# Kernel tuning notes

Hardware: AMD Instinct MI355X
Metric: run time of the kernel (lower is better)

## Reference

```python
import jax, jax.numpy as jnp
import numpy as np

N = 100000
D = 256
E = 1600000
H, C = 2, 32  # heads, out_channels


def setup_inputs() -> dict:
    key = jax.random.key(0)
    ks = jax.random.split(key, 10)
    h_x = jax.random.normal(ks[0], (N, D), dtype=jnp.float32)
    t_x = jax.random.normal(ks[1], (N, D), dtype=jnp.float32)
    src = jax.random.randint(ks[2], (E,), 0, N, dtype=jnp.int32)
    off = jax.random.randint(ks[3], (E,), 1, N, dtype=jnp.int32)
    dst = (src + off) % N  # guarantees src != dst (remove_self_loops is a no-op)
    edge_index = jnp.stack([src, dst])  # [2, E]
    enrichment_weights = jax.random.uniform(ks[4], (E,), dtype=jnp.float32) * 3.0
    s = 1.0 / np.sqrt(D)
    W_src = jax.random.normal(ks[5], (D, H * C), dtype=jnp.float32) * s
    W_dst = jax.random.normal(ks[6], (D, H * C), dtype=jnp.float32) * s
    att_src = jax.random.normal(ks[7], (H, C), dtype=jnp.float32) * 0.1
    att_dst = jax.random.normal(ks[8], (H, C), dtype=jnp.float32) * 0.1
    bias = jnp.zeros((H * C,), dtype=jnp.float32)
    enrichment_scale = jnp.float32(0.5)
    return {"h_x": h_x, "t_x": t_x, "edge_index": edge_index,
            "enrichment_weights": enrichment_weights,
            "W_src": W_src, "W_dst": W_dst, "att_src": att_src,
            "att_dst": att_dst, "bias": bias,
            "enrichment_scale": enrichment_scale}


def _gat(x_src, x_dst, src, dst, num_dst, W_src, W_dst, att_src, att_dst, bias):
    # PyG GATConv, bipartite, heads=H, out=C, concat=True, eval mode
    hs = (x_src @ W_src).reshape(-1, H, C)  # [Ns, H, C]
    hd = (x_dst @ W_dst).reshape(-1, H, C)  # [Nd, H, C]
    a_s = jnp.einsum('nhc,hc->nh', hs, att_src)  # [Ns, H]
    a_d = jnp.einsum('nhc,hc->nh', hd, att_dst)  # [Nd, H]
    alpha = jax.nn.leaky_relu(a_s[src] + a_d[dst], 0.2)  # [E', H]
    m = jax.ops.segment_max(alpha, dst, num_segments=num_dst)
    alpha = jnp.exp(alpha - m[dst])
    z = jax.ops.segment_sum(alpha, dst, num_segments=num_dst)
    alpha = alpha / (z[dst] + 1e-16)
    msg = hs[src] * alpha[:, :, None]  # [E', H, C]
    out = jax.ops.segment_sum(msg, dst, num_segments=num_dst)  # [Nd, H, C]
    return out.reshape(num_dst, H * C) + bias


def reference(h_x, t_x, edge_index, enrichment_weights,
              W_src, W_dst, att_src, att_dst, bias, enrichment_scale):
    h_in = jax.nn.elu(h_x)
    t_in = jax.nn.elu(t_x)
    src, dst = edge_index[0], edge_index[1]
    loops = jnp.arange(min(h_x.shape[0], t_x.shape[0]), dtype=src.dtype)
    # direction 1: (h -> t), PyG appends self-loops after the input edges
    s1 = jnp.concatenate([src, loops]); d1 = jnp.concatenate([dst, loops])
    t_rep = _gat(h_in, t_in, s1, d1, t_x.shape[0], W_src, W_dst, att_src, att_dst, bias)
    # direction 2: reversed edges (t -> h)
    s2 = jnp.concatenate([dst, loops]); d2 = jnp.concatenate([src, loops])
    h_rep = _gat(t_in, h_in, s2, d2, h_x.shape[0], W_src, W_dst, att_src, att_dst, bias)
    # edge-enrichment reweighting (scalar factor)
    scale = 0.5 * jnp.tanh(enrichment_scale)
    ew = jnp.clip(enrichment_weights, 0.3, 3.0)
    aw = jax.nn.softmax(ew)
    weighted = jnp.sum(aw * ew)
    factor = 1.0 + scale * (weighted - 1.0)
    return (h_rep * factor, t_rep * factor)
```

## Files before the change

kernel.cpp:

```cpp
#include <hip/hip_runtime.h>
#include <hip/hip_fp16.h>
#include <math.h>

typedef __attribute__((ext_vector_type(8))) short bf16x8;
typedef __attribute__((ext_vector_type(4))) float f32x4;

__device__ __forceinline__ float bf2f(unsigned short u) {
    union { unsigned int i; float f; } c;
    c.i = ((unsigned int)u) << 16;
    return c.f;
}
__device__ __forceinline__ unsigned short f2bf(float f) {
    union { float f; unsigned int i; } c;
    c.f = f;
    unsigned int b = c.i + 0x7FFFu + ((c.i >> 16) & 1u);
    return (unsigned short)(b >> 16);
}
__device__ __forceinline__ float eluf(float v) {
    return v > 0.f ? v : (__expf(v) - 1.f);
}
__device__ __forceinline__ float lrelu(float v) {
    return v >= 0.f ? v : 0.2f * v;
}
__device__ __forceinline__ unsigned int fenc(float f) {
    union { float f; unsigned int u; } c; c.f = f;
    return (c.u & 0x80000000u) ? ~c.u : (c.u | 0x80000000u);
}
__device__ __forceinline__ float fdec(unsigned int k) {
    union { float f; unsigned int u; } c;
    c.u = (k & 0x80000000u) ? (k ^ 0x80000000u) : ~k;
    return c.f;
}

__global__ void detect_kernel(const unsigned int* __restrict__ w, int nwords,
                              int* __restrict__ flag)
{
    __shared__ int cnt_s;
    if (threadIdx.x == 0) cnt_s = 0;
    __syncthreads();
    int sane = 0;
    for (int i = threadIdx.x; i < nwords; i += 256) {
        unsigned int lo = w[i] & 0xffffu;
        int e = (int)((lo >> 7) & 0xffu);
        if (e >= 114 && e <= 136) sane++;
    }
    atomicAdd(&cnt_s, sane);
    __syncthreads();
    if (threadIdx.x == 0) *flag = (2 * cnt_s > nwords) ? 1 : 0;
}

__global__ __launch_bounds__(256) void wfrag_kernel(
    const unsigned short* __restrict__ Wsrc, const unsigned short* __restrict__ Wdst,
    const int* __restrict__ flag, unsigned short* __restrict__ Wfrag)
{
    if (!*flag) return;
    const int nch = 8 * 8 * 64;
    for (int ch = blockIdx.x * 256 + threadIdx.x; ch < nch; ch += gridDim.x * 256) {
        int l  = ch & 63;
        int t  = (ch >> 6) & 7;
        int ks = ch >> 9;
        int col = t * 16 + (l & 15);
        int k0  = ks * 32 + (l >> 4) * 8;
        const unsigned short* W = (col < 64) ? (Wsrc + col) : (Wdst + (col - 64));
#pragma unroll
        for (int j = 0; j < 8; ++j)
            Wfrag[(size_t)ch * 8 + j] = W[(size_t)(k0 + j) * 64];
    }
}

__global__ __launch_bounds__(256) void gemm_mfma_kernel(
    const void* __restrict__ xh, const void* __restrict__ xt,
    const unsigned short* __restrict__ Wfrag,
    const void* __restrict__ att_src, const void* __restrict__ att_dst,
    const int* __restrict__ flag,
    __half* __restrict__ P, float* __restrict__ as_all, float* __restrict__ ad_all,
    int N)
{
    if (!*flag) return;
    const unsigned short* xv = (const unsigned short*)((blockIdx.y == 0) ? xh : xt);
    __half* Pout = P + (size_t)blockIdx.y * (size_t)N * 64u;
    float* asO  = as_all + (size_t)blockIdx.y * (size_t)N * 2u;
    float* adO  = ad_all + (size_t)blockIdx.y * (size_t)N * 2u;
    const int tid = threadIdx.x;
    const int w   = tid >> 6;
    const int l   = tid & 63;
    const int l15 = l & 15;
    const int lhi = l >> 4;
    const int rowA = blockIdx.x * 64 + w * 16 + l15;
    const bool rv = rowA < N;

    bf16x8 a[8];
#pragma unroll
    for (int ks = 0; ks < 8; ++ks) {
        union { bf16x8 v; unsigned int u[4]; } o;
        if (rv) {
            uint4 raw = *(const uint4*)(xv + (size_t)rowA * 256 + ks * 32 + lhi * 8);
            unsigned int wsr[4] = {raw.x, raw.y, raw.z, raw.w};
#pragma unroll
            for (int i = 0; i < 4; ++i) {
                float lo = eluf(bf2f((unsigned short)(wsr[i] & 0xffffu)));
                float hi = eluf(bf2f((unsigned short)(wsr[i] >> 16)));
                o.u[i] = (unsigned int)f2bf(lo) | ((unsigned int)f2bf(hi) << 16);
            }
        } else {
            o.u[0] = o.u[1] = o.u[2] = o.u[3] = 0u;
        }
        a[ks] = o.v;
    }

    f32x4 acc[8];
#pragma unroll
    for (int t = 0; t < 8; ++t) acc[t] = (f32x4){0.f, 0.f, 0.f, 0.f};

    const bf16x8* wf = (const bf16x8*)Wfrag;
#pragma unroll
    for (int ks = 0; ks < 8; ++ks) {
#pragma unroll
        for (int t = 0; t < 8; ++t) {
            bf16x8 b = wf[(ks * 8 + t) * 64 + l];
            acc[t] = __builtin_amdgcn_mfma_f32_16x16x32_bf16(a[ks], b, acc[t], 0, 0, 0);
        }
    }

    float asv[4], adv[4];
#pragma unroll
    for (int t = 0; t < 4; ++t) {
        asv[t] = bf2f(((const unsigned short*)att_src)[t * 16 + l15]);
        adv[t] = bf2f(((const unsigned short*)att_dst)[t * 16 + l15]);
    }
    const int rbase = blockIdx.x * 64 + w * 16 + lhi * 4;
#pragma unroll
    for (int reg = 0; reg < 4; ++reg) {
        int row = rbase + reg;
        bool ok = row < N;
        if (ok) {
            __half* p = Pout + (size_t)row * 64 + l15;
#pragma unroll
            for (int t = 0; t < 4; ++t) p[t * 16] = __float2half(acc[t][reg]);
        }
        float s0 = acc[0][reg] * asv[0] + acc[1][reg] * asv[1];
        float s1 = acc[2][reg] * asv[2] + acc[3][reg] * asv[3];
        float d0 = acc[4][reg] * adv[0] + acc[5][reg] * adv[1];
        float d1 = acc[6][reg] * adv[2] + acc[7][reg] * adv[3];
#pragma unroll
        for (int o2 = 8; o2 >= 1; o2 >>= 1) {
            s0 += __shfl_xor(s0, o2, 64);
            s1 += __shfl_xor(s1, o2, 64);
            d0 += __shfl_xor(d0, o2, 64);
            d1 += __shfl_xor(d1, o2, 64);
        }
        if (ok && l15 == 0) {
            asO[(size_t)row * 2 + 0] = s0;
            asO[(size_t)row * 2 + 1] = s1;
            adO[(size_t)row * 2 + 0] = d0;
            adO[(size_t)row * 2 + 1] = d1;
        }
    }
}

__global__ __launch_bounds__(256) void gemm_elu_kernel(
    const void* __restrict__ xh, const void* __restrict__ xt,
    const void* __restrict__ Wsrc, const void* __restrict__ Wdst,
    const void* __restrict__ att_src, const void* __restrict__ att_dst,
    const int* __restrict__ flag,
    __half* __restrict__ P, float* __restrict__ as_all, float* __restrict__ ad_all,
    int N, int D, int skip_bf)
{
    const int isbf = *flag;
    if (skip_bf && isbf) return;
    __shared__ float xs[64][33];
    __shared__ float wt[32][128];
    const void* xv = (blockIdx.y == 0) ? xh : xt;
    __half* Pout = P + (size_t)blockIdx.y * (size_t)N * 64u;
    float* asO  = as_all + (size_t)blockIdx.y * (size_t)N * 2u;
    float* adO  = ad_all + (size_t)blockIdx.y * (size_t)N * 2u;
    const int rowBase = blockIdx.x * 64;
    const int tid = threadIdx.x;
    const int tcx = tid & 15;
    const int tcy = tid >> 4;

    float acc[4][8];
#pragma unroll
    for (int r = 0; r < 4; ++r)
#pragma unroll
        for (int c = 0; c < 8; ++c) acc[r][c] = 0.f;

    for (int kc = 0; kc < D; kc += 32) {
        {
            int row = tid >> 2;
            int kq  = (tid & 3) * 8;
            int r = rowBase + row;
            float v[8];
            if (r < N) {
                if (isbf) {
                    const unsigned short* xb = (const unsigned short*)xv;
                    uint4 raw = *(const uint4*)(xb + (size_t)r * D + kc + kq);
                    unsigned int ws[4] = {raw.x, raw.y, raw.z, raw.w};
#pragma unroll
                    for (int i = 0; i < 4; ++i) {
                        v[2 * i]     = bf2f((unsigned short)(ws[i] & 0xffffu));
                        v[2 * i + 1] = bf2f((unsigned short)(ws[i] >> 16));
                    }
                } else {
                    const float* xf = (const float*)xv;
                    const float4* p4 = (const float4*)(xf + (size_t)r * D + kc + kq);
                    float4 f0 = p4[0], f1 = p4[1];
                    v[0] = f0.x; v[1] = f0.y; v[2] = f0.z; v[3] = f0.w;
                    v[4] = f1.x; v[5] = f1.y; v[6] = f1.z; v[7] = f1.w;
                }
#pragma unroll
                for (int i = 0; i < 8; ++i) v[i] = eluf(v[i]);
            } else {
#pragma unroll
                for (int i = 0; i < 8; ++i) v[i] = 0.f;
            }
#pragma unroll
            for (int i = 0; i < 8; ++i) xs[row][kq + i] = v[i];
        }
#pragma unroll
        for (int i = 0; i < 2; ++i) {
            int f = (tid + i * 256) * 8;
            int k = f >> 7;
            int c = f & 127;
            float v[8];
            if (isbf) {
                const unsigned short* Wp = (c < 64)
                    ? ((const unsigned short*)Wsrc + (size_t)(kc + k) * 64 + c)
                    : ((const unsigned short*)Wdst + (size_t)(kc + k) * 64 + (c - 64));
                uint4 raw = *(const uint4*)Wp;
                unsigned int ws[4] = {raw.x, raw.y, raw.z, raw.w};
#pragma unroll
                for (int q = 0; q < 4; ++q) {
                    v[2 * q]     = bf2f((unsigned short)(ws[q] & 0xffffu));
                    v[2 * q + 1] = bf2f((unsigned short)(ws[q] >> 16));
                }
            } else {
                const float* Wp = (c < 64)
                    ? ((const float*)Wsrc + (size_t)(kc + k) * 64 + c)
                    : ((const float*)Wdst + (size_t)(kc + k) * 64 + (c - 64));
                const float4* p4 = (const float4*)Wp;
                float4 f0 = p4[0], f1 = p4[1];
                v[0] = f0.x; v[1] = f0.y; v[2] = f0.z; v[3] = f0.w;
                v[4] = f1.x; v[5] = f1.y; v[6] = f1.z; v[7] = f1.w;
            }
#pragma unroll
            for (int q = 0; q < 8; ++q) wt[k][c + q] = v[q];
        }
        __syncthreads();
#pragma unroll 8
        for (int k = 0; k < 32; ++k) {
            float xr[4];
#pragma unroll
            for (int r = 0; r < 4; ++r) xr[r] = xs[tcy * 4 + r][k];
            float4 w0 = *(const float4*)&wt[k][tcx * 8];
            float4 w1 = *(const float4*)&wt[k][tcx * 8 + 4];
#pragma unroll
            for (int r = 0; r < 4; ++r) {
                acc[r][0] += xr[r] * w0.x; acc[r][1] += xr[r] * w0.y;
                acc[r][2] += xr[r] * w0.z; acc[r][3] += xr[r] * w0.w;
                acc[r][4] += xr[r] * w1.x; acc[r][5] += xr[r] * w1.y;
                acc[r][6] += xr[r] * w1.z; acc[r][7] += xr[r] * w1.w;
            }
        }
        __syncthreads();
    }

    float attv[8];
#pragma unroll
    for (int q = 0; q < 8; ++q) {
        int c = tcx * 8 + q;
        if (isbf) attv[q] = (c < 64) ? bf2f(((const unsigned short*)att_src)[c])
                                     : bf2f(((const unsigned short*)att_dst)[c - 64]);
        else      attv[q] = (c < 64) ? ((const float*)att_src)[c]
                                     : ((const float*)att_dst)[c - 64];
    }

#pragma unroll
    for (int r = 0; r < 4; ++r) {
        int row = rowBase + tcy * 4 + r;
        bool ok = row < N;
        if (ok && tcx < 8) {
            __half* p = Pout + (size_t)row * 64 + tcx * 8;
#pragma unroll
            for (int q = 0; q < 8; ++q) p[q] = __float2half(acc[r][q]);
        }
        float part = 0.f;
#pragma unroll
        for (int q = 0; q < 8; ++q) part += acc[r][q] * attv[q];
        part += __shfl_xor(part, 1, 64);
        part += __shfl_xor(part, 2, 64);
        if (ok && (tcx & 3) == 0) {
            if (tcx == 0)       asO[(size_t)row * 2 + 0] = part;
            else if (tcx == 4)  asO[(size_t)row * 2 + 1] = part;
            else if (tcx == 8)  adO[(size_t)row * 2 + 0] = part;
            else                adO[(size_t)row * 2 + 1] = part;
        }
    }
}

__global__ __launch_bounds__(256) void gmax_kernel(
    const float* __restrict__ as_all, unsigned int* __restrict__ gmax, int N)
{
    unsigned int k0 = 0, k1 = 0, k2 = 0, k3 = 0;
    const int total = 2 * N;
    for (int i = blockIdx.x * 256 + threadIdx.x; i < total; i += gridDim.x * 256) {
        float2 v = *(const float2*)(as_all + (size_t)i * 2);
        unsigned int ex = fenc(v.x), ey = fenc(v.y);
        if (i < N) { k0 = max(k0, ex); k1 = max(k1, ey); }
        else       { k2 = max(k2, ex); k3 = max(k3, ey); }
    }
#pragma unroll
    for (int o = 32; o >= 1; o >>= 1) {
        k0 = max(k0, (unsigned int)__shfl_xor((int)k0, o, 64));
        k1 = max(k1, (unsigned int)__shfl_xor((int)k1, o, 64));
        k2 = max(k2, (unsigned int)__shfl_xor((int)k2, o, 64));
        k3 = max(k3, (unsigned int)__shfl_xor((int)k3, o, 64));
    }
    if ((threadIdx.x & 63) == 0) {
        atomicMax(&gmax[0], k0);
        atomicMax(&gmax[1], k1);
        atomicMax(&gmax[2], k2);
        atomicMax(&gmax[3], k3);
    }
}

__global__ void count_kernel(const int* __restrict__ srce, const int* __restrict__ dste,
                             int* __restrict__ cnt, int N, int E)
{
    int e = blockIdx.x * blockDim.x + threadIdx.x;
    if (e >= E) return;
    atomicAdd(&cnt[dste[e]], 1);
    atomicAdd(&cnt[N + srce[e]], 1);
}

__global__ __launch_bounds__(256) void scan_bsum_kernel(
    const int* __restrict__ cnt, int M, int chunk, int* __restrict__ bsum)
{
    __shared__ int r[4];
    int beg = blockIdx.x * chunk;
    int end = beg + chunk; if (end > M) end = M;
    int s = 0;
    for (int i = beg + threadIdx.x; i < end; i += 256) s += cnt[i];
#pragma unroll
    for (int o = 32; o >= 1; o >>= 1) s += __shfl_down(s, o, 64);
    int lane = threadIdx.x & 63, wv = threadIdx.x >> 6;
    if (lane == 0) r[wv] = s;
    __syncthreads();
    if (threadIdx.x == 0) bsum[blockIdx.x] = r[0] + r[1] + r[2] + r[3];
}

__global__ __launch_bounds__(256) void scan_boff_kernel(
    const int* __restrict__ bsum, int NB, int* __restrict__ boff)
{
    __shared__ int s[256];
    int t = threadIdx.x;
    int v = (t < NB) ? bsum[t] : 0;
    s[t] = v;
    __syncthreads();
    for (int o = 1; o < 256; o <<= 1) {
        int x = (t >= o) ? s[t - o] : 0;
        __syncthreads();
        s[t] += x;
        __syncthreads();
    }
    if (t < NB) boff[t] = s[t] - v;
}

__global__ __launch_bounds__(256) void scan_write_kernel(
    const int* __restrict__ cnt, int M, int chunk,
    const int* __restrict__ boff, int* __restrict__ off)
{
    __shared__ int s[256];
    int t = threadIdx.x;
    int beg = blockIdx.x * chunk;
    int end = beg + chunk; if (end > M) end = M;
    if (beg >= M) return;
    int running = boff[blockIdx.x];
    for (int base = beg; base < end; base += 256) {
        int i = base + t;
        int v = (i < end) ? cnt[i] : 0;
        s[t] = v;
        __syncthreads();
        for (int o = 1; o < 256; o <<= 1) {
            int x = (t >= o) ? s[t - o] : 0;
            __syncthreads();
            s[t] += x;
            __syncthreads();
        }
        if (i < end) off[i] = running + s[t] - v;
        int total = s[255];
        __syncthreads();
        running += total;
    }
    if (end == M && t == 0) off[M] = running;
}

__global__ void fill_kernel(const int* __restrict__ srce, const int* __restrict__ dste,
                            const int* __restrict__ off, int* __restrict__ cur,
                            int* __restrict__ idx, int N, int E)
{
    int e = blockIdx.x * blockDim.x + threadIdx.x;
    if (e >= E) return;
    int s = srce[e], d = dste[e];
    int p  = atomicAdd(&cur[d], 1);
    idx[off[d] + p] = s;
    int p2 = atomicAdd(&cur[N + s], 1);
    idx[off[N + s] + p2] = d;
}

__global__ __launch_bounds__(256) void enrich_kernel(
    const void* __restrict__ ew, const int* __restrict__ flag,
    float* __restrict__ S, int E)
{
    __shared__ float r1[4], r2[4];
    const int isbf = *flag;
    float e1 = 0.f, e2 = 0.f;
    for (int i = blockIdx.x * 256 + threadIdx.x; i < E; i += gridDim.x * 256) {
        float c = isbf ? bf2f(((const unsigned short*)ew)[i]) : ((const float*)ew)[i];
        c = fminf(fmaxf(c, 0.3f), 3.0f);
        float ex = __expf(c);
        e1 += ex;
        e2 += c * ex;
    }
#pragma unroll
    for (int o = 32; o >= 1; o >>= 1) {
        e1 += __shfl_down(e1, o, 64);
        e2 += __shfl_down(e2, o, 64);
    }
    int lane = threadIdx.x & 63;
    int wv = threadIdx.x >> 6;
    if (lane == 0) { r1[wv] = e1; r2[wv] = e2; }
    __syncthreads();
    if (threadIdx.x == 0) {
        atomicAdd(&S[0], r1[0] + r1[1] + r1[2] + r1[3]);
        atomicAdd(&S[1], r2[0] + r2[1] + r2[2] + r2[3]);
    }
}

__global__ __launch_bounds__(256) void agg_kernel(
    const int* __restrict__ off, const int* __restrict__ idx,
    const float* __restrict__ as_all, const float* __restrict__ ad_all,
    const __half* __restrict__ Pall,
    const void* __restrict__ bias,
    const float* __restrict__ S,
    const unsigned int* __restrict__ gmax,
    const void* __restrict__ esc,
    const int* __restrict__ flag,
    void* __restrict__ out, int N)
{
    const int isbf = *flag;
    int q = (blockIdx.x * 256 + threadIdx.x) >> 6;
    int lane = threadIdx.x & 63;
    if (q >= 2 * N) return;
    int dir = (q >= N) ? 1 : 0;
    int n = q - dir * N;
    const float* a_s  = as_all + (size_t)dir * 2u * (size_t)N;
    const float* a_d  = ad_all + (size_t)(1 - dir) * 2u * (size_t)N;
    const __half* Psrc = Pall + (size_t)dir * (size_t)N * 64u;
    size_t outOff = dir ? 0u : (size_t)N * 64u;
    const int hi = lane >> 5;
    const int jb = off[q], je = off[q + 1];

    float2 adv2 = *(const float2*)(a_d + (size_t)n * 2);
    const float adv = hi ? adv2.y : adv2.x;
    const float gm  = fdec(gmax[dir * 2 + hi]);
    const float m   = lrelu(gm + adv);

    float2 ass2 = *(const float2*)(a_s + (size_t)n * 2);
    const float pSelf = __expf(lrelu((hi ? ass2.y : ass2.x) + adv) - m);
    float z0 = pSelf, z1 = 0.f;
    float acc0 = pSelf * __half2float(Psrc[(size_t)n * 64 + lane]);
    float acc1 = 0.f;

    int j = jb;
    for (; j + 1 < je; j += 2) {
        int s0 = idx[j], s1 = idx[j + 1];
        float2 a0 = *(const float2*)(a_s + (size_t)s0 * 2);
        float2 a1 = *(const float2*)(a_s + (size_t)s1 * 2);
        float h0 = __half2float(Psrc[(size_t)s0 * 64 + lane]);
        float h1 = __half2float(Psrc[(size_t)s1 * 64 + lane]);
        float p0 = __expf(lrelu((hi ? a0.y : a0.x) + adv) - m);
        float p1 = __expf(lrelu((hi ? a1.y : a1.x) + adv) - m);
        z0 += p0; acc0 = fmaf(p0, h0, acc0);
        z1 += p1; acc1 = fmaf(p1, h1, acc1);
    }
    if (j < je) {
        int s0 = idx[j];
        float2 a0 = *(const float2*)(a_s + (size_t)s0 * 2);
        float h0 = __half2float(Psrc[(size_t)s0 * 64 + lane]);
        float p0 = __expf(lrelu((hi ? a0.y : a0.x) + adv) - m);
        z0 += p0; acc0 = fmaf(p0, h0, acc0);
    }
    float z   = z0 + z1;
    float acc = acc0 + acc1;

    float escv = isbf ? bf2f(((const unsigned short*)esc)[0]) : ((const float*)esc)[0];
    float bv   = isbf ? bf2f(((const unsigned short*)bias)[lane]) : ((const float*)bias)[lane];
    float weighted = S[1] / S[0];
    float factor = 1.f + 0.5f * tanhf(escv) * (weighted - 1.f);
    float o = (acc / (z + 1e-16f) + bv) * factor;
    size_t oi = outOff + (size_t)n * 64 + lane;
    if (isbf) ((unsigned short*)out)[oi] = f2bf(o);
    else      ((float*)out)[oi] = o;
}

extern "C" void kernel_launch(void* const* d_in, const int* in_sizes, int n_in,
                              void* d_out, int out_size, void* d_ws, size_t ws_size,
                              hipStream_t stream)
{
    const void* hx      = d_in[0];
    const void* tx      = d_in[1];
    const int*  eidx    = (const int*)d_in[2];
    const void* ew      = d_in[3];
    const void* Wsrc    = d_in[4];
    const void* Wdst    = d_in[5];
    const void* att_src = d_in[6];
    const void* att_dst = d_in[7];
    const void* bias    = d_in[8];
    const void* esc     = d_in[9];

    const int HC = in_sizes[6];
    const int D  = in_sizes[4] / HC;
    const int N  = in_sizes[0] / D;
    const int E  = in_sizes[3];
    const int* srce = eidx;
    const int* dste = eidx + E;

    const bool canM = (D == 256) && (HC == 64);
    const int skipBf = canM ? 1 : 0;

    char* wsb = (char*)d_ws;
    size_t o = 0;
    auto alloc = [&](size_t bytes) -> void* {
        void* p = wsb + o;
        o += (bytes + 255) & ~(size_t)255;
        return p;
    };
    __half* Pall  = (__half*)alloc((size_t)2 * N * 64 * 2);
    float* as_all = (float*)alloc((size_t)2 * N * 2 * 4);
    float* ad_all = (float*)alloc((size_t)2 * N * 2 * 4);
    float* S      = (float*)alloc(2 * 4);
    unsigned int* gmax = (unsigned int*)alloc(4 * 4);
    int*   cnt    = (int*)alloc((size_t)2 * N * 4);
    int*   offp   = (int*)alloc(((size_t)2 * N + 1) * 4);
    int*   cur    = (int*)alloc((size_t)2 * N * 4);
    int*   idx    = (int*)alloc((size_t)2 * E * 4);
    int*   flag   = (int*)alloc(256);
    int*   bsum   = (int*)alloc(256 * 4);
    int*   boff   = (int*)alloc(256 * 4);
    unsigned short* Wfrag = (unsigned short*)alloc((size_t)8 * 8 * 64 * 8 * 2);

    hipMemsetAsync(cnt, 0, (size_t)2 * N * 4, stream);
    hipMemsetAsync(cur, 0, (size_t)2 * N * 4, stream);
    hipMemsetAsync(S, 0, 2 * 4, stream);
    hipMemsetAsync(gmax, 0, 4 * 4, stream);

    detect_kernel<<<1, 256, 0, stream>>>((const unsigned int*)hx, 65536, flag);

    dim3 gGemm((N + 63) / 64, 2);
    if (canM) {
        wfrag_kernel<<<16, 256, 0, stream>>>((const unsigned short*)Wsrc,
                                             (const unsigned short*)Wdst, flag, Wfrag);
        gemm_mfma_kernel<<<gGemm, 256, 0, stream>>>(hx, tx, Wfrag, att_src, att_dst,
                                                    flag, Pall, as_all, ad_all, N);
    }
    gemm_elu_kernel<<<gGemm, 256, 0, stream>>>(hx, tx, Wsrc, Wdst, att_src, att_dst,
                                               flag, Pall, as_all, ad_all, N, D, skipBf);
    gmax_kernel<<<256, 256, 0, stream>>>(as_all, gmax, N);
    count_kernel<<<(E + 255) / 256, 256, 0, stream>>>(srce, dste, cnt, N, E);

    const int M = 2 * N;
    int chunk = (M + 255) / 256;
    chunk = (chunk + 255) & ~255;
    const int NB = (M + chunk - 1) / chunk;
    scan_bsum_kernel<<<NB, 256, 0, stream>>>(cnt, M, chunk, bsum);
    scan_boff_kernel<<<1, 256, 0, stream>>>(bsum, NB, boff);
    scan_write_kernel<<<NB, 256, 0, stream>>>(cnt, M, chunk, boff, offp);

    fill_kernel<<<(E + 255) / 256, 256, 0, stream>>>(srce, dste, offp, cur, idx, N, E);
    enrich_kernel<<<512, 256, 0, stream>>>(ew, flag, S, E);

    agg_kernel<<<(2 * N + 3) / 4, 256, 0, stream>>>(offp, idx, as_all, ad_all,
                                                    Pall, bias, S, gmax, esc, flag,
                                                    d_out, N);
}
```

Baseline: 1.008 ms.

## Route fp32 GEMM through split-bf16 MFMA with hi/lo error compensation

The fp32 input path now uses the MFMA kernel instead of the shared-memory FMA GEMM. Activations and weights are split into bf16 high and low parts, and three MFMAs (hi*hi, lo*hi, hi*lo) recover near-fp32 accuracy. The scalar tiled GEMM for the 2x100000x256x128 projection is meant to be replaced by matrix cores. The cost is three times the MFMA work, an extra weight-fragment buffer, and a small loss of precision against a true fp32 product.

```diff
diff --git a/kernel.cpp b/kernel.cpp
--- a/kernel.cpp
+++ b/kernel.cpp
@@ -50,10 +50,11 @@
 }
 
 __global__ __launch_bounds__(256) void wfrag_kernel(
-    const unsigned short* __restrict__ Wsrc, const unsigned short* __restrict__ Wdst,
-    const int* __restrict__ flag, unsigned short* __restrict__ Wfrag)
-{
-    if (!*flag) return;
+    const void* __restrict__ Wsrc, const void* __restrict__ Wdst,
+    const int* __restrict__ flag,
+    unsigned short* __restrict__ Whi, unsigned short* __restrict__ Wlo)
+{
+    const int isbf = *flag;
     const int nch = 8 * 8 * 64;
     for (int ch = blockIdx.x * 256 + threadIdx.x; ch < nch; ch += gridDim.x * 256) {
         int l  = ch & 63;
@@ -61,23 +62,39 @@
         int ks = ch >> 9;
         int col = t * 16 + (l & 15);
         int k0  = ks * 32 + (l >> 4) * 8;
-        const unsigned short* W = (col < 64) ? (Wsrc + col) : (Wdst + (col - 64));
-#pragma unroll
-        for (int j = 0; j < 8; ++j)
-            Wfrag[(size_t)ch * 8 + j] = W[(size_t)(k0 + j) * 64];
-    }
-}
-
-__global__ __launch_bounds__(256) void gemm_mfma_kernel(
+        if (isbf) {
+            const unsigned short* W = (col < 64)
+                ? ((const unsigned short*)Wsrc + col)
+                : ((const unsigned short*)Wdst + (col - 64));
+#pragma unroll
+            for (int j = 0; j < 8; ++j) {
+                Whi[(size_t)ch * 8 + j] = W[(size_t)(k0 + j) * 64];
+                Wlo[(size_t)ch * 8 + j] = 0;
+            }
+        } else {
+            const float* W = (col < 64)
+                ? ((const float*)Wsrc + col)
+                : ((const float*)Wdst + (col - 64));
+#pragma unroll
+            for (int j = 0; j < 8; ++j) {
+                float wv = W[(size_t)(k0 + j) * 64];
+                unsigned short h = f2bf(wv);
+                Whi[(size_t)ch * 8 + j] = h;
+                Wlo[(size_t)ch * 8 + j] = f2bf(wv - bf2f(h));
+            }
+        }
+    }
+}
+
+__global__ __launch_bounds__(256) void gemm_fused_kernel(
     const void* __restrict__ xh, const void* __restrict__ xt,
-    const unsigned short* __restrict__ Wfrag,
+    const unsigned short* __restrict__ Whi, const unsigned short* __restrict__ Wlo,
     const void* __restrict__ att_src, const void* __restrict__ att_dst,
     const int* __restrict__ flag,
     __half* __restrict__ P, float* __restrict__ as_all, float* __restrict__ ad_all,
     int N)
 {
-    if (!*flag) return;
-    const unsigned short* xv = (const unsigned short*)((blockIdx.y == 0) ? xh : xt);
+    const int isbf = *flag;
     __half* Pout = P + (size_t)blockIdx.y * (size_t)N * 64u;
     float* asO  = as_all + (size_t)blockIdx.y * (size_t)N * 2u;
     float* adO  = ad_all + (size_t)blockIdx.y * (size_t)N * 2u;
@@ -89,44 +106,95 @@
     const int rowA = blockIdx.x * 64 + w * 16 + l15;
     const bool rv = rowA < N;
 
-    bf16x8 a[8];
-#pragma unroll
-    for (int ks = 0; ks < 8; ++ks) {
-        union { bf16x8 v; unsigned int u[4]; } o;
-        if (rv) {
-            uint4 raw = *(const uint4*)(xv + (size_t)rowA * 256 + ks * 32 + lhi * 8);
-            unsigned int wsr[4] = {raw.x, raw.y, raw.z, raw.w};
-#pragma unroll
-            for (int i = 0; i < 4; ++i) {
-                float lo = eluf(bf2f((unsigned short)(wsr[i] & 0xffffu)));
-                float hi = eluf(bf2f((unsigned short)(wsr[i] >> 16)));
-                o.u[i] = (unsigned int)f2bf(lo) | ((unsigned int)f2bf(hi) << 16);
-            }
+    bf16x8 ahi[8], alo[8];
+    if (isbf) {
+        const unsigned short* xv = (const unsigned short*)((blockIdx.y == 0) ? xh : xt);
+#pragma unroll
+        for (int ks = 0; ks < 8; ++ks) {
+            union { bf16x8 v; unsigned int u[4]; } o;
+            if (rv) {
+                uint4 raw = *(const uint4*)(xv + (size_t)rowA * 256 + ks * 32 + lhi * 8);
+                unsigned int wsr[4] = {raw.x, raw.y, raw.z, raw.w};
+#pragma unroll
+                for (int i = 0; i < 4; ++i) {
+                    float lo = eluf(bf2f((unsigned short)(wsr[i] & 0xffffu)));
+                    float hi = eluf(bf2f((unsigned short)(wsr[i] >> 16)));
+                    o.u[i] = (unsigned int)f2bf(lo) | ((unsigned int)f2bf(hi) << 16);
+                }
+            } else {
+                o.u[0] = o.u[1] = o.u[2] = o.u[3] = 0u;
+            }
+            ahi[ks] = o.v;
+            alo[ks] = o.v;
+        }
+    } else {
+        const float* xv = (const float*)((blockIdx.y == 0) ? xh : xt);
+#pragma unroll
+        for (int ks = 0; ks < 8; ++ks) {
+            union { bf16x8 v; unsigned int u[4]; } oh, ol;
+            if (rv) {
+                const float4* px = (const float4*)(xv + (size_t)rowA * 256 + ks * 32 + lhi * 8);
+                float4 f0 = px[0], f1 = px[1];
+                float v[8] = {f0.x, f0.y, f0.z, f0.w, f1.x, f1.y, f1.z, f1.w};
+#pragma unroll
+                for (int i = 0; i < 8; ++i) v[i] = eluf(v[i]);
+#pragma unroll
+                for (int i = 0; i < 4; ++i) {
+                    unsigned short h0 = f2bf(v[2 * i]);
+                    unsigned short h1 = f2bf(v[2 * i + 1]);
+                    unsigned short l0 = f2bf(v[2 * i]     - bf2f(h0));
+                    unsigned short l1 = f2bf(v[2 * i + 1] - bf2f(h1));
+                    oh.u[i] = (unsigned int)h0 | ((unsigned int)h1 << 16);
+                    ol.u[i] = (unsigned int)l0 | ((unsigned int)l1 << 16);
+                }
+            } else {
+                oh.u[0] = oh.u[1] = oh.u[2] = oh.u[3] = 0u;
+                ol.u[0] = ol.u[1] = ol.u[2] = ol.u[3] = 0u;
+            }
+            ahi[ks] = oh.v;
+            alo[ks] = ol.v;
+        }
+    }
+
+    f32x4 acc[8];
+#pragma unroll
+    for (int t = 0; t < 8; ++t) acc[t] = (f32x4){0.f, 0.f, 0.f, 0.f};
+
+    const bf16x8* wfh = (const bf16x8*)Whi;
+    const bf16x8* wfl = (const bf16x8*)Wlo;
+    if (isbf) {
+#pragma unroll
+        for (int ks = 0; ks < 8; ++ks) {
+#pragma unroll
+            for (int t = 0; t < 8; ++t) {
+                bf16x8 b = wfh[(ks * 8 + t) * 64 + l];
+                acc[t] = __builtin_amdgcn_mfma_f32_16x16x32_bf16(ahi[ks], b, acc[t], 0, 0, 0);
+            }
+        }
+    } else {
+#pragma unroll
+        for (int ks = 0; ks < 8; ++ks) {
+#pragma unroll
+            for (int t = 0; t < 8; ++t) {
+                bf16x8 bh = wfh[(ks * 8 + t) * 64 + l];
+                bf16x8 bl = wfl[(ks * 8 + t) * 64 + l];
+                acc[t] = __builtin_amdgcn_mfma_f32_16x16x32_bf16(ahi[ks], bh, acc[t], 0, 0, 0);
+                acc[t] = __builtin_amdgcn_mfma_f32_16x16x32_bf16(alo[ks], bh, acc[t], 0, 0, 0);
+                acc[t] = __builtin_amdgcn_mfma_f32_16x16x32_bf16(ahi[ks], bl, acc[t], 0, 0, 0);
+            }
+        }
+    }
+
+    float asv[4], adv[4];
+#pragma unroll
+    for (int t = 0; t < 4; ++t) {
+        if (isbf) {
+            asv[t] = bf2f(((const unsigned short*)att_src)[t * 16 + l15]);
+            adv[t] = bf2f(((const unsigned short*)att_dst)[t * 16 + l15]);
         } else {
-            o.u[0] = o.u[1] = o.u[2] = o.u[3] = 0u;
-        }
-        a[ks] = o.v;
-    }
-
-    f32x4 acc[8];
-#pragma unroll
-    for (int t = 0; t < 8; ++t) acc[t] = (f32x4){0.f, 0.f, 0.f, 0.f};
-
-    const bf16x8* wf = (const bf16x8*)Wfrag;
-#pragma unroll
-    for (int ks = 0; ks < 8; ++ks) {
-#pragma unroll
-        for (int t = 0; t < 8; ++t) {
-            bf16x8 b = wf[(ks * 8 + t) * 64 + l];
-            acc[t] = __builtin_amdgcn_mfma_f32_16x16x32_bf16(a[ks], b, acc[t], 0, 0, 0);
-        }
-    }
-
-    float asv[4], adv[4];
-#pragma unroll
-    for (int t = 0; t < 4; ++t) {
-        asv[t] = bf2f(((const unsigned short*)att_src)[t * 16 + l15]);
-        adv[t] = bf2f(((const unsigned short*)att_dst)[t * 16 + l15]);
+            asv[t] = ((const float*)att_src)[t * 16 + l15];
+            adv[t] = ((const float*)att_dst)[t * 16 + l15];
+        }
     }
     const int rbase = blockIdx.x * 64 + w * 16 + lhi * 4;
 #pragma unroll
@@ -164,10 +232,9 @@
     const void* __restrict__ att_src, const void* __restrict__ att_dst,
     const int* __restrict__ flag,
     __half* __restrict__ P, float* __restrict__ as_all, float* __restrict__ ad_all,
-    int N, int D, int skip_bf)
+    int N, int D)
 {
     const int isbf = *flag;
-    if (skip_bf && isbf) return;
     __shared__ float xs[64][33];
     __shared__ float wt[32][128];
     const void* xv = (blockIdx.y == 0) ? xh : xt;
@@ -527,7 +594,6 @@
     const int* dste = eidx + E;
 
     const bool canM = (D == 256) && (HC == 64);
-    const int skipBf = canM ? 1 : 0;
 
     char* wsb = (char*)d_ws;
     size_t o = 0;
@@ -548,7 +614,8 @@
     int*   flag   = (int*)alloc(256);
     int*   bsum   = (int*)alloc(256 * 4);
     int*   boff   = (int*)alloc(256 * 4);
-    unsigned short* Wfrag = (unsigned short*)alloc((size_t)8 * 8 * 64 * 8 * 2);
+    unsigned short* Whi = (unsigned short*)alloc((size_t)8 * 8 * 64 * 8 * 2);
+    unsigned short* Wlo = (unsigned short*)alloc((size_t)8 * 8 * 64 * 8 * 2);
 
     hipMemsetAsync(cnt, 0, (size_t)2 * N * 4, stream);
     hipMemsetAsync(cur, 0, (size_t)2 * N * 4, stream);
@@ -559,13 +626,14 @@
 
     dim3 gGemm((N + 63) / 64, 2);
     if (canM) {
-        wfrag_kernel<<<16, 256, 0, stream>>>((const unsigned short*)Wsrc,
-                                             (const unsigned short*)Wdst, flag, Wfrag);
-        gemm_mfma_kernel<<<gGemm, 256, 0, stream>>>(hx, tx, Wfrag, att_src, att_dst,
-                                                    flag, Pall, as_all, ad_all, N);
-    }
-    gemm_elu_kernel<<<gGemm, 256, 0, stream>>>(hx, tx, Wsrc, Wdst, att_src, att_dst,
-                                               flag, Pall, as_all, ad_all, N, D, skipBf);
+        wfrag_kernel<<<16, 256, 0, stream>>>(Wsrc, Wdst, flag, Whi, Wlo);
+        gemm_fused_kernel<<<gGemm, 256, 0, stream>>>(hx, tx, Whi, Wlo,
+                                                     att_src, att_dst, flag,
+                                                     Pall, as_all, ad_all, N);
+    } else {
+        gemm_elu_kernel<<<gGemm, 256, 0, stream>>>(hx, tx, Wsrc, Wdst, att_src, att_dst,
+                                                   flag, Pall, as_all, ad_all, N, D);
+    }
     gmax_kernel<<<256, 256, 0, stream>>>(as_all, gmax, N);
     count_kernel<<<(E + 255) / 256, 256, 0, stream>>>(srce, dste, cnt, N, E);
 
```

After: 960.0 us. 1.05x faster.
